# Performance work log

Measured on AMD Instinct MI355X. Metric: run time of the kernel, lower is better.

The kernel has to match this reference:

```python
import jax, jax.numpy as jnp
import numpy as np

IN_DIM = 768
HID = 128
NUM_CLASSES = 32
N_NODES = 50000
N_EDGES = 1600000


def setup_inputs() -> dict:
    key = jax.random.key(0)
    ks = jax.random.split(key, 8)
    x = jax.random.normal(ks[0], (N_NODES, IN_DIM), dtype=jnp.float32)
    edge_index = jax.random.randint(ks[1], (2, N_EDGES), 0, N_NODES, dtype=jnp.int64)
    # GCNConv weights (PyG: linear without bias inside propagate, bias added after aggregation)
    W1 = jax.random.normal(ks[2], (IN_DIM, HID), dtype=jnp.float32) / np.sqrt(IN_DIM)
    b1 = jnp.zeros((HID,), dtype=jnp.float32)
    W2 = jax.random.normal(ks[3], (HID, HID), dtype=jnp.float32) / np.sqrt(HID)
    b2 = jnp.zeros((HID,), dtype=jnp.float32)
    Wfc = jax.random.normal(ks[4], (HID, NUM_CLASSES), dtype=jnp.float32) / np.sqrt(HID)
    bfc = jnp.zeros((NUM_CLASSES,), dtype=jnp.float32)
    return {"x": x, "edge_index": edge_index, "W1": W1, "b1": b1,
            "W2": W2, "b2": b2, "Wfc": Wfc, "bfc": bfc}


def _gcn_conv(x, src, dst, norm, W, b, num_nodes):
    # PyG GCNConv: h = x @ W; out[i] = sum_j norm_ij * h[j]; out += b
    h = x @ W                      # [N, out_dim]
    msgs = h[src] * norm[:, None]  # gather + scale, [E+N, out_dim]
    out = jax.ops.segment_sum(msgs, dst, num_segments=num_nodes)
    return out + b


def reference(x, edge_index, W1, b1, W2, b2, Wfc, bfc):
    n = x.shape[0]
    loop = jnp.arange(n, dtype=edge_index.dtype)
    src = jnp.concatenate([edge_index[0], loop])  # add self-loops
    dst = jnp.concatenate([edge_index[1], loop])
    # symmetric normalization: deg computed on destination with unit edge weights
    deg = jax.ops.segment_sum(jnp.ones_like(src, dtype=x.dtype), dst, num_segments=n)
    dinv = jnp.where(deg > 0, jax.lax.rsqrt(jnp.maximum(deg, 1.0)), 0.0)
    norm = dinv[src] * dinv[dst]  # [E+N]

    h = jax.nn.relu(_gcn_conv(x, src, dst, norm, W1, b1, n))
    h = jax.nn.relu(_gcn_conv(h, src, dst, norm, W2, b2, n))
    return h @ Wfc + bfc
```

## Files before the change

kernel.cpp:

```cpp
#include <hip/hip_runtime.h>
#include <hip/hip_bf16.h>
#include <hip/hip_fp16.h>

#define N_NODES 50000
#define IN_DIM 768
#define HID 128
#define NCLS 32
#define CHUNK 8192
#define NBUCK ((N_NODES + 255) >> 8)

typedef __attribute__((ext_vector_type(8))) short bf16x8;
typedef __attribute__((ext_vector_type(4))) float f32x4;
typedef __attribute__((ext_vector_type(4))) unsigned short u16x4;

__device__ inline void split_bf16(float x, unsigned short& hi, unsigned short& lo) {
    unsigned int u = __float_as_uint(x);
    hi = (unsigned short)(u >> 16);
    float r = x - __uint_as_float(u & 0xFFFF0000u);
    lo = (unsigned short)(__float_as_uint(r) >> 16);
}

__global__ __launch_bounds__(256) void count_bucket(const int* __restrict__ raw, int E,
                                                    int* __restrict__ hist) {
    __shared__ int cnt[NBUCK];
    bool is64 = (raw[1] == 0 && raw[3] == 0 && raw[5] == 0 && raw[7] == 0);
    int t = threadIdx.x, b = blockIdx.x;
    if (t < NBUCK) cnt[t] = 0;
    __syncthreads();
    int base = b * CHUNK;
#pragma unroll
    for (int j = 0; j < CHUNK / 256; ++j) {
        int e = base + j * 256 + t;
        if (e < E) {
            int d = is64 ? raw[2 * (E + e)] : raw[E + e];
            atomicAdd(&cnt[d >> 8], 1);
        }
    }
    __syncthreads();
    if (t < NBUCK) hist[b * NBUCK + t] = cnt[t];
}

__global__ __launch_bounds__(256) void scan_off2(const int* __restrict__ hist, int nblk,
                                                 int E, int* __restrict__ bstart,
                                                 int* __restrict__ off) {
    __shared__ int tot[256];
    int t = threadIdx.x;
    int sum = 0;
    if (t < NBUCK)
        for (int b = 0; b < nblk; ++b) sum += hist[b * NBUCK + t];
    tot[t] = (t < NBUCK) ? sum : 0;
    __syncthreads();
    for (int o = 1; o < 256; o <<= 1) {
        int v = (t >= o) ? tot[t - o] : 0;
        __syncthreads();
        tot[t] += v;
        __syncthreads();
    }
    int excl = (t == 0) ? 0 : tot[t - 1];
    if (t < NBUCK) {
        bstart[t] = excl;
        int run = excl;
        for (int b = 0; b < nblk; ++b) {
            off[b * NBUCK + t] = run;
            run += hist[b * NBUCK + t];
        }
    }
    if (t == 0) bstart[NBUCK] = E;
}

__global__ __launch_bounds__(256) void chunk_scatter(const int* __restrict__ raw, int E,
                                                     const int* __restrict__ off,
                                                     int2* __restrict__ ebuf) {
    __shared__ int offl[NBUCK];
    __shared__ int cnt[NBUCK];
    bool is64 = (raw[1] == 0 && raw[3] == 0 && raw[5] == 0 && raw[7] == 0);
    int t = threadIdx.x, b = blockIdx.x;
    if (t < NBUCK) { offl[t] = off[b * NBUCK + t]; cnt[t] = 0; }
    __syncthreads();
    int base = b * CHUNK;
#pragma unroll
    for (int j = 0; j < CHUNK / 256; ++j) {
        int e = base + j * 256 + t;
        if (e < E) {
            int s, d;
            if (is64) { s = raw[2 * e]; d = raw[2 * (E + e)]; }
            else      { s = raw[e];     d = raw[E + e]; }
            int k = d >> 8;
            int r = atomicAdd(&cnt[k], 1);
            ebuf[offl[k] + r] = make_int2(s, d);
        }
    }
}

__global__ __launch_bounds__(256) void bucket_fine2(const int2* __restrict__ ebuf,
                                                    const int* __restrict__ bstart,
                                                    int* __restrict__ rowp,
                                                    float* __restrict__ dinv,
                                                    int* __restrict__ csr, int n, int E) {
    __shared__ int cnt[256];
    __shared__ int pre[256];
    __shared__ int fil[256];
    int k = blockIdx.x, t = threadIdx.x;
    int base = k << 8;
    int nn = min(256, n - base);
    int es = bstart[k], ee = bstart[k + 1];
    cnt[t] = 0;
    __syncthreads();
    for (int p = es + t; p < ee; p += 256) atomicAdd(&cnt[ebuf[p].y - base], 1);
    __syncthreads();
    pre[t] = cnt[t];
    __syncthreads();
    for (int o = 1; o < 256; o <<= 1) {
        int v = (t >= o) ? pre[t - o] : 0;
        __syncthreads();
        pre[t] += v;
        __syncthreads();
    }
    int excl = (t == 0) ? 0 : pre[t - 1];
    if (t < nn) {
        rowp[base + t] = es + excl;
        dinv[base + t] = rsqrtf((float)(cnt[t] + 1));
    }
    if (k == gridDim.x - 1 && t == 0) rowp[n] = E;
    fil[t] = es + excl;
    __syncthreads();
    for (int p = es + t; p < ee; p += 256) {
        int2 sd = ebuf[p];
        int q = atomicAdd(&fil[sd.y - base], 1);
        csr[q] = sd.x;
    }
}

__global__ void pack_w(const float* __restrict__ W, int K,
                       unsigned short* __restrict__ ph, unsigned short* __restrict__ pl) {
    int gid = blockIdx.x * 256 + threadIdx.x;
    int total = (K / 32) * 8 * 64;
    if (gid >= total) return;
    int l = gid & 63;
    int c0 = (gid >> 6) & 7;
    int t = gid >> 9;
    int col = c0 * 16 + (l & 15);
    int k0 = t * 32 + ((l >> 4) << 3);
    size_t base = (size_t)gid * 8;
#pragma unroll
    for (int j = 0; j < 8; ++j) {
        unsigned short h, lo;
        split_bf16(W[(size_t)(k0 + j) * 128 + col], h, lo);
        ph[base + j] = h;
        pl[base + j] = lo;
    }
}

template <int K>
__global__ __launch_bounds__(256) void gemm_mfma2(const float* __restrict__ A,
                                                  const unsigned short* __restrict__ Bph,
                                                  const unsigned short* __restrict__ Bpl,
                                                  __half* __restrict__ Chalf, int M) {
    __shared__ unsigned short Ah[64][40];
    __shared__ unsigned short Al[64][40];
    int tid = threadIdx.x;
    int wid = tid >> 6, lane = tid & 63;
    int wr = wid >> 1, wc = wid & 1;
    int row0 = blockIdx.x * 64;
    int lrow = lane & 15, lk = (lane >> 4) * 8;
    const int T = K / 32;

    int sidx0 = tid, sidx1 = 256 + tid;
    int sr0 = sidx0 >> 3, sc0 = (sidx0 & 7) * 4;
    int sr1 = sidx1 >> 3, sc1 = (sidx1 & 7) * 4;
    bool v0 = (row0 + sr0) < M, v1 = (row0 + sr1) < M;
    const float* a0 = &A[(size_t)(row0 + sr0) * K + sc0];
    const float* a1 = &A[(size_t)(row0 + sr1) * K + sc1];

    float4 pre0 = make_float4(0.f, 0.f, 0.f, 0.f), pre1 = pre0;
    if (v0) pre0 = *(const float4*)a0;
    if (v1) pre1 = *(const float4*)a1;

    f32x4 acc[2][4] = {};
    for (int t = 0; t < T; ++t) {
        u16x4 h, lo;
        split_bf16(pre0.x, ((unsigned short*)&h)[0], ((unsigned short*)&lo)[0]);
        split_bf16(pre0.y, ((unsigned short*)&h)[1], ((unsigned short*)&lo)[1]);
        split_bf16(pre0.z, ((unsigned short*)&h)[2], ((unsigned short*)&lo)[2]);
        split_bf16(pre0.w, ((unsigned short*)&h)[3], ((unsigned short*)&lo)[3]);
        *(u16x4*)&Ah[sr0][sc0] = h;
        *(u16x4*)&Al[sr0][sc0] = lo;
        split_bf16(pre1.x, ((unsigned short*)&h)[0], ((unsigned short*)&lo)[0]);
        split_bf16(pre1.y, ((unsigned short*)&h)[1], ((unsigned short*)&lo)[1]);
        split_bf16(pre1.z, ((unsigned short*)&h)[2], ((unsigned short*)&lo)[2]);
        split_bf16(pre1.w, ((unsigned short*)&h)[3], ((unsigned short*)&lo)[3]);
        *(u16x4*)&Ah[sr1][sc1] = h;
        *(u16x4*)&Al[sr1][sc1] = lo;
        __syncthreads();
        if (t + 1 < T) {
            pre0 = make_float4(0.f, 0.f, 0.f, 0.f); pre1 = pre0;
            if (v0) pre0 = *(const float4*)(a0 + (t + 1) * 32);
            if (v1) pre1 = *(const float4*)(a1 + (t + 1) * 32);
        }
        bf16x8 ah[2], al[2];
#pragma unroll
        for (int m = 0; m < 2; ++m) {
            int r = wr * 32 + m * 16 + lrow;
            ah[m] = *(const bf16x8*)&Ah[r][lk];
            al[m] = *(const bf16x8*)&Al[r][lk];
        }
        bf16x8 bh[4], bl[4];
#pragma unroll
        for (int n = 0; n < 4; ++n) {
            size_t boff = ((size_t)(t * 8 + wc * 4 + n) * 64 + lane) * 8;
            bh[n] = *(const bf16x8*)&Bph[boff];
            bl[n] = *(const bf16x8*)&Bpl[boff];
        }
#pragma unroll
        for (int m = 0; m < 2; ++m)
#pragma unroll
            for (int n = 0; n < 4; ++n) {
                acc[m][n] = __builtin_amdgcn_mfma_f32_16x16x32_bf16(ah[m], bh[n], acc[m][n], 0, 0, 0);
                acc[m][n] = __builtin_amdgcn_mfma_f32_16x16x32_bf16(al[m], bh[n], acc[m][n], 0, 0, 0);
                acc[m][n] = __builtin_amdgcn_mfma_f32_16x16x32_bf16(ah[m], bl[n], acc[m][n], 0, 0, 0);
            }
        __syncthreads();
    }
#pragma unroll
    for (int m = 0; m < 2; ++m) {
        int rbase = row0 + wr * 32 + m * 16 + (lane >> 4) * 4;
#pragma unroll
        for (int n = 0; n < 4; ++n) {
            int col = wc * 64 + n * 16 + lrow;
#pragma unroll
            for (int j = 0; j < 4; ++j) {
                int r = rbase + j;
                if (r < M) Chalf[(size_t)r * 128 + col] = __float2half(acc[m][n][j]);
            }
        }
    }
}

__global__ __launch_bounds__(256) void aggregate3(const __half* __restrict__ ht,
                                                  const int* __restrict__ rowp,
                                                  const int* __restrict__ csr,
                                                  const float* __restrict__ dinv,
                                                  const float* __restrict__ bias,
                                                  float* __restrict__ out, int n) {
    int wid = threadIdx.x >> 6, lane = threadIdx.x & 63;
    int i = blockIdx.x * 4 + wid;
    if (i >= n) return;
    const __half2* h2 = (const __half2*)ht;
    float di = dinv[i];
    float2 self = __half22float2(h2[(size_t)i * 64 + lane]);
    float2 acc;
    acc.x = di * di * self.x;
    acc.y = di * di * self.y;
    int b = rowp[i], e = rowp[i + 1];
    int p = b;
    for (; p + 8 <= e; p += 8) {
        int s[8]; float2 v[8]; float nn[8];
#pragma unroll
        for (int q = 0; q < 8; ++q) s[q] = csr[p + q];
#pragma unroll
        for (int q = 0; q < 8; ++q) v[q] = __half22float2(h2[(size_t)s[q] * 64 + lane]);
#pragma unroll
        for (int q = 0; q < 8; ++q) nn[q] = dinv[s[q]] * di;
#pragma unroll
        for (int q = 0; q < 8; ++q) { acc.x += nn[q] * v[q].x; acc.y += nn[q] * v[q].y; }
    }
    for (; p < e; ++p) {
        int s = csr[p];
        float nn = dinv[s] * di;
        float2 v = __half22float2(h2[(size_t)s * 64 + lane]);
        acc.x += nn * v.x;
        acc.y += nn * v.y;
    }
    float2 bb = ((const float2*)bias)[lane];
    float2 o;
    o.x = fmaxf(acc.x + bb.x, 0.f);
    o.y = fmaxf(acc.y + bb.y, 0.f);
    ((float2*)out)[(size_t)i * 64 + lane] = o;
}

__global__ __launch_bounds__(256) void fc_out(const float* __restrict__ h,
                                              const float* __restrict__ W,
                                              const float* __restrict__ b,
                                              float* __restrict__ out, int n) {
    __shared__ float Ws[HID * NCLS];
    __shared__ float Hs[8][HID];
    int tid = threadIdx.x;
#pragma unroll
    for (int l = 0; l < 16; ++l) Ws[l * 256 + tid] = W[l * 256 + tid];
    int row0 = blockIdx.x * 8;
#pragma unroll
    for (int l = 0; l < 4; ++l) {
        int idx = l * 256 + tid;
        int r = idx >> 7, c = idx & 127;
        int gr = row0 + r;
        Hs[r][c] = (gr < n) ? h[(size_t)gr * HID + c] : 0.f;
    }
    __syncthreads();
    int r = tid >> 5, c = tid & 31;
    float acc = b[c];
#pragma unroll
    for (int k = 0; k < HID; ++k) acc += Hs[r][k] * Ws[k * NCLS + c];
    int gr = row0 + r;
    if (gr < n) out[(size_t)gr * NCLS + c] = acc;
}

extern "C" void kernel_launch(void* const* d_in, const int* in_sizes, int n_in,
                              void* d_out, int out_size, void* d_ws, size_t ws_size,
                              hipStream_t stream) {
    const float* x   = (const float*)d_in[0];
    const int*   eid = (const int*)d_in[1];
    const float* W1  = (const float*)d_in[2];
    const float* b1  = (const float*)d_in[3];
    const float* W2  = (const float*)d_in[4];
    const float* b2  = (const float*)d_in[5];
    const float* Wfc = (const float*)d_in[6];
    const float* bfc = (const float*)d_in[7];
    float* out = (float*)d_out;

    const int N = N_NODES;
    const int E = in_sizes[1] / 2;
    const int NBLK = (E + CHUNK - 1) / CHUNK;

    auto align = [](size_t v) { return (v + 255) & ~(size_t)255; };
    char* w = (char*)d_ws;
    size_t off = 0;
    int* rowp = (int*)(w + off);           off = align(off + (size_t)(N + 1) * 4);
    float* dinv = (float*)(w + off);       off = align(off + (size_t)N * 4);
    int* csr = (int*)(w + off);            off = align(off + (size_t)E * 4);
    int2* ebuf = (int2*)(w + off);         off = align(off + (size_t)E * 8);
    int* bstart = (int*)(w + off);         off = align(off + (size_t)(NBUCK + 1) * 4);
    int* hist = (int*)(w + off);           off = align(off + (size_t)NBLK * NBUCK * 4);
    int* offs = (int*)(w + off);           off = align(off + (size_t)NBLK * NBUCK * 4);
    unsigned short* W1ph = (unsigned short*)(w + off); off = align(off + (size_t)128 * IN_DIM * 2);
    unsigned short* W1pl = (unsigned short*)(w + off); off = align(off + (size_t)128 * IN_DIM * 2);
    unsigned short* W2ph = (unsigned short*)(w + off); off = align(off + (size_t)128 * HID * 2);
    unsigned short* W2pl = (unsigned short*)(w + off); off = align(off + (size_t)128 * HID * 2);
    __half* h1 = (__half*)(w + off);       off = align(off + (size_t)N * HID * 2);
    __half* h2t = (__half*)(w + off);      off = align(off + (size_t)N * HID * 2);
    float* bufA = (float*)(w + off);       off = align(off + (size_t)N * HID * 4);
    float* bufB = (float*)(w + off);       off = align(off + (size_t)N * HID * 4);

    count_bucket<<<NBLK, 256, 0, stream>>>(eid, E, hist);
    scan_off2<<<1, 256, 0, stream>>>(hist, NBLK, E, bstart, offs);
    chunk_scatter<<<NBLK, 256, 0, stream>>>(eid, E, offs, ebuf);
    bucket_fine2<<<NBUCK, 256, 0, stream>>>(ebuf, bstart, rowp, dinv, csr, N, E);

    pack_w<<<((IN_DIM / 32) * 8 * 64 + 255) / 256, 256, 0, stream>>>(W1, IN_DIM, W1ph, W1pl);
    pack_w<<<((HID / 32) * 8 * 64 + 255) / 256, 256, 0, stream>>>(W2, HID, W2ph, W2pl);

    int gb = (N + 63) / 64;
    gemm_mfma2<IN_DIM><<<gb, 256, 0, stream>>>(x, W1ph, W1pl, h1, N);
    aggregate3<<<(N + 3) / 4, 256, 0, stream>>>(h1, rowp, csr, dinv, b1, bufA, N);
    gemm_mfma2<HID><<<gb, 256, 0, stream>>>(bufA, W2ph, W2pl, h2t, N);
    aggregate3<<<(N + 3) / 4, 256, 0, stream>>>(h2t, rowp, csr, dinv, b2, bufB, N);
    fc_out<<<(N + 7) / 8, 256, 0, stream>>>(bufB, Wfc, bfc, out, N);
}
```

Before: 313.6 us.

## Fold dinv into GEMM epilogue, compress CSR to 16-bit, use half intermediates

The GEMM epilogue now pre-scales each output row by dinv[src]. Aggregation therefore sums raw gathered rows and applies dinv[dst] once, with no per-edge dinv gather or multiply. The edge buffer packs the local destination and the source into 32 bits, CSR indices become uint16 since node ids fit in 16 bits, and the inner gather loop is unrolled to 16. Intermediate activations between layers are stored as fp16 instead of fp32, and the second GEMM and the final FC read half input. This reduces memory traffic, at the cost of extra fp16 rounding and a hard limit of 65536 nodes.

```diff
diff --git a/kernel.cpp b/kernel.cpp
--- a/kernel.cpp
+++ b/kernel.cpp
@@ -70,7 +70,7 @@
 
 __global__ __launch_bounds__(256) void chunk_scatter(const int* __restrict__ raw, int E,
                                                      const int* __restrict__ off,
-                                                     int2* __restrict__ ebuf) {
+                                                     unsigned int* __restrict__ ebuf) {
     __shared__ int offl[NBUCK];
     __shared__ int cnt[NBUCK];
     bool is64 = (raw[1] == 0 && raw[3] == 0 && raw[5] == 0 && raw[7] == 0);
@@ -87,16 +87,17 @@
             else      { s = raw[e];     d = raw[E + e]; }
             int k = d >> 8;
             int r = atomicAdd(&cnt[k], 1);
-            ebuf[offl[k] + r] = make_int2(s, d);
-        }
-    }
-}
-
-__global__ __launch_bounds__(256) void bucket_fine2(const int2* __restrict__ ebuf,
+            ebuf[offl[k] + r] = ((unsigned int)(d & 255) << 16) | (unsigned int)s;
+        }
+    }
+}
+
+__global__ __launch_bounds__(256) void bucket_fine2(const unsigned int* __restrict__ ebuf,
                                                     const int* __restrict__ bstart,
                                                     int* __restrict__ rowp,
                                                     float* __restrict__ dinv,
-                                                    int* __restrict__ csr, int n, int E) {
+                                                    unsigned short* __restrict__ csr,
+                                                    int n, int E) {
     __shared__ int cnt[256];
     __shared__ int pre[256];
     __shared__ int fil[256];
@@ -106,7 +107,7 @@
     int es = bstart[k], ee = bstart[k + 1];
     cnt[t] = 0;
     __syncthreads();
-    for (int p = es + t; p < ee; p += 256) atomicAdd(&cnt[ebuf[p].y - base], 1);
+    for (int p = es + t; p < ee; p += 256) atomicAdd(&cnt[ebuf[p] >> 16], 1);
     __syncthreads();
     pre[t] = cnt[t];
     __syncthreads();
@@ -125,9 +126,9 @@
     fil[t] = es + excl;
     __syncthreads();
     for (int p = es + t; p < ee; p += 256) {
-        int2 sd = ebuf[p];
-        int q = atomicAdd(&fil[sd.y - base], 1);
-        csr[q] = sd.x;
+        unsigned int u = ebuf[p];
+        int q = atomicAdd(&fil[u >> 16], 1);
+        csr[q] = (unsigned short)(u & 0xFFFFu);
     }
 }
 
@@ -151,10 +152,23 @@
     }
 }
 
-template <int K>
-__global__ __launch_bounds__(256) void gemm_mfma2(const float* __restrict__ A,
+template <bool AHALF>
+__device__ inline float4 loadA4(const void* A, size_t idx) {
+    if constexpr (AHALF) {
+        uint2 u = *(const uint2*)((const __half*)A + idx);
+        float2 f0 = __half22float2(*(__half2*)&u.x);
+        float2 f1 = __half22float2(*(__half2*)&u.y);
+        return make_float4(f0.x, f0.y, f1.x, f1.y);
+    } else {
+        return *(const float4*)((const float*)A + idx);
+    }
+}
+
+template <int K, bool AHALF>
+__global__ __launch_bounds__(256) void gemm_mfma2(const void* __restrict__ A,
                                                   const unsigned short* __restrict__ Bph,
                                                   const unsigned short* __restrict__ Bpl,
+                                                  const float* __restrict__ dinv,
                                                   __half* __restrict__ Chalf, int M) {
     __shared__ unsigned short Ah[64][40];
     __shared__ unsigned short Al[64][40];
@@ -169,12 +183,12 @@
     int sr0 = sidx0 >> 3, sc0 = (sidx0 & 7) * 4;
     int sr1 = sidx1 >> 3, sc1 = (sidx1 & 7) * 4;
     bool v0 = (row0 + sr0) < M, v1 = (row0 + sr1) < M;
-    const float* a0 = &A[(size_t)(row0 + sr0) * K + sc0];
-    const float* a1 = &A[(size_t)(row0 + sr1) * K + sc1];
+    size_t ai0 = (size_t)(row0 + sr0) * K + sc0;
+    size_t ai1 = (size_t)(row0 + sr1) * K + sc1;
 
     float4 pre0 = make_float4(0.f, 0.f, 0.f, 0.f), pre1 = pre0;
-    if (v0) pre0 = *(const float4*)a0;
-    if (v1) pre1 = *(const float4*)a1;
+    if (v0) pre0 = loadA4<AHALF>(A, ai0);
+    if (v1) pre1 = loadA4<AHALF>(A, ai1);
 
     f32x4 acc[2][4] = {};
     for (int t = 0; t < T; ++t) {
@@ -194,8 +208,8 @@
         __syncthreads();
         if (t + 1 < T) {
             pre0 = make_float4(0.f, 0.f, 0.f, 0.f); pre1 = pre0;
-            if (v0) pre0 = *(const float4*)(a0 + (t + 1) * 32);
-            if (v1) pre1 = *(const float4*)(a1 + (t + 1) * 32);
+            if (v0) pre0 = loadA4<AHALF>(A, ai0 + (size_t)(t + 1) * 32);
+            if (v1) pre1 = loadA4<AHALF>(A, ai1 + (size_t)(t + 1) * 32);
         }
         bf16x8 ah[2], al[2];
 #pragma unroll
@@ -230,55 +244,56 @@
 #pragma unroll
             for (int j = 0; j < 4; ++j) {
                 int r = rbase + j;
-                if (r < M) Chalf[(size_t)r * 128 + col] = __float2half(acc[m][n][j]);
+                if (r < M) Chalf[(size_t)r * 128 + col] = __float2half(dinv[r] * acc[m][n][j]);
             }
         }
     }
 }
 
-__global__ __launch_bounds__(256) void aggregate3(const __half* __restrict__ ht,
+__global__ __launch_bounds__(256) void aggregate5(const __half* __restrict__ ht,
                                                   const int* __restrict__ rowp,
-                                                  const int* __restrict__ csr,
+                                                  const unsigned short* __restrict__ csr,
                                                   const float* __restrict__ dinv,
                                                   const float* __restrict__ bias,
-                                                  float* __restrict__ out, int n) {
+                                                  __half* __restrict__ outh, int n) {
     int wid = threadIdx.x >> 6, lane = threadIdx.x & 63;
     int i = blockIdx.x * 4 + wid;
     if (i >= n) return;
     const __half2* h2 = (const __half2*)ht;
     float di = dinv[i];
-    float2 self = __half22float2(h2[(size_t)i * 64 + lane]);
-    float2 acc;
-    acc.x = di * di * self.x;
-    acc.y = di * di * self.y;
+    float2 acc = __half22float2(h2[(size_t)i * 64 + lane]);
     int b = rowp[i], e = rowp[i + 1];
     int p = b;
-    for (; p + 8 <= e; p += 8) {
-        int s[8]; float2 v[8]; float nn[8];
-#pragma unroll
-        for (int q = 0; q < 8; ++q) s[q] = csr[p + q];
-#pragma unroll
-        for (int q = 0; q < 8; ++q) v[q] = __half22float2(h2[(size_t)s[q] * 64 + lane]);
-#pragma unroll
-        for (int q = 0; q < 8; ++q) nn[q] = dinv[s[q]] * di;
-#pragma unroll
-        for (int q = 0; q < 8; ++q) { acc.x += nn[q] * v[q].x; acc.y += nn[q] * v[q].y; }
+    for (; p + 16 <= e; p += 16) {
+        int s[16]; float2 v[16];
+#pragma unroll
+        for (int q = 0; q < 16; ++q) s[q] = csr[p + q];
+#pragma unroll
+        for (int q = 0; q < 16; ++q) v[q] = __half22float2(h2[(size_t)s[q] * 64 + lane]);
+#pragma unroll
+        for (int q = 0; q < 16; ++q) { acc.x += v[q].x; acc.y += v[q].y; }
+    }
+    for (; p + 4 <= e; p += 4) {
+        int s[4]; float2 v[4];
+#pragma unroll
+        for (int q = 0; q < 4; ++q) s[q] = csr[p + q];
+#pragma unroll
+        for (int q = 0; q < 4; ++q) v[q] = __half22float2(h2[(size_t)s[q] * 64 + lane]);
+#pragma unroll
+        for (int q = 0; q < 4; ++q) { acc.x += v[q].x; acc.y += v[q].y; }
     }
     for (; p < e; ++p) {
-        int s = csr[p];
-        float nn = dinv[s] * di;
-        float2 v = __half22float2(h2[(size_t)s * 64 + lane]);
-        acc.x += nn * v.x;
-        acc.y += nn * v.y;
+        float2 v = __half22float2(h2[(size_t)csr[p] * 64 + lane]);
+        acc.x += v.x;
+        acc.y += v.y;
     }
     float2 bb = ((const float2*)bias)[lane];
-    float2 o;
-    o.x = fmaxf(acc.x + bb.x, 0.f);
-    o.y = fmaxf(acc.y + bb.y, 0.f);
-    ((float2*)out)[(size_t)i * 64 + lane] = o;
-}
-
-__global__ __launch_bounds__(256) void fc_out(const float* __restrict__ h,
+    __half2 o = __floats2half2_rn(fmaxf(di * acc.x + bb.x, 0.f),
+                                  fmaxf(di * acc.y + bb.y, 0.f));
+    ((__half2*)outh)[(size_t)i * 64 + lane] = o;
+}
+
+__global__ __launch_bounds__(256) void fc_out(const __half* __restrict__ h,
                                               const float* __restrict__ W,
                                               const float* __restrict__ b,
                                               float* __restrict__ out, int n) {
@@ -293,7 +308,7 @@
         int idx = l * 256 + tid;
         int r = idx >> 7, c = idx & 127;
         int gr = row0 + r;
-        Hs[r][c] = (gr < n) ? h[(size_t)gr * HID + c] : 0.f;
+        Hs[r][c] = (gr < n) ? __half2float(h[(size_t)gr * HID + c]) : 0.f;
     }
     __syncthreads();
     int r = tid >> 5, c = tid & 31;
@@ -326,8 +341,8 @@
     size_t off = 0;
     int* rowp = (int*)(w + off);           off = align(off + (size_t)(N + 1) * 4);
     float* dinv = (float*)(w + off);       off = align(off + (size_t)N * 4);
-    int* csr = (int*)(w + off);            off = align(off + (size_t)E * 4);
-    int2* ebuf = (int2*)(w + off);         off = align(off + (size_t)E * 8);
+    unsigned short* csr = (unsigned short*)(w + off); off = align(off + (size_t)E * 2);
+    unsigned int* ebuf = (unsigned int*)(w + off);    off = align(off + (size_t)E * 4);
     int* bstart = (int*)(w + off);         off = align(off + (size_t)(NBUCK + 1) * 4);
     int* hist = (int*)(w + off);           off = align(off + (size_t)NBLK * NBUCK * 4);
     int* offs = (int*)(w + off);           off = align(off + (size_t)NBLK * NBUCK * 4);
@@ -335,10 +350,10 @@
     unsigned short* W1pl = (unsigned short*)(w + off); off = align(off + (size_t)128 * IN_DIM * 2);
     unsigned short* W2ph = (unsigned short*)(w + off); off = align(off + (size_t)128 * HID * 2);
     unsigned short* W2pl = (unsigned short*)(w + off); off = align(off + (size_t)128 * HID * 2);
-    __half* h1 = (__half*)(w + off);       off = align(off + (size_t)N * HID * 2);
-    __half* h2t = (__half*)(w + off);      off = align(off + (size_t)N * HID * 2);
-    float* bufA = (float*)(w + off);       off = align(off + (size_t)N * HID * 4);
-    float* bufB = (float*)(w + off);       off = align(off + (size_t)N * HID * 4);
+    __half* ht1 = (__half*)(w + off);      off = align(off + (size_t)N * HID * 2);
+    __half* ht2 = (__half*)(w + off);      off = align(off + (size_t)N * HID * 2);
+    __half* h1r = (__half*)(w + off);      off = align(off + (size_t)N * HID * 2);
+    __half* h2r = (__half*)(w + off);      off = align(off + (size_t)N * HID * 2);
 
     count_bucket<<<NBLK, 256, 0, stream>>>(eid, E, hist);
     scan_off2<<<1, 256, 0, stream>>>(hist, NBLK, E, bstart, offs);
@@ -349,9 +364,10 @@
     pack_w<<<((HID / 32) * 8 * 64 + 255) / 256, 256, 0, stream>>>(W2, HID, W2ph, W2pl);
 
     int gb = (N + 63) / 64;
-    gemm_mfma2<IN_DIM><<<gb, 256, 0, stream>>>(x, W1ph, W1pl, h1, N);
-    aggregate3<<<(N + 3) / 4, 256, 0, stream>>>(h1, rowp, csr, dinv, b1, bufA, N);
-    gemm_mfma2<HID><<<gb, 256, 0, stream>>>(bufA, W2ph, W2pl, h2t, N);
-    aggregate3<<<(N + 3) / 4, 256, 0, stream>>>(h2t, rowp, csr, dinv, b2, bufB, N);
-    fc_out<<<(N + 7) / 8, 256, 0, stream>>>(bufB, Wfc, bfc, out, N);
-}
+    int ab = (N + 3) / 4;
+    gemm_mfma2<IN_DIM, false><<<gb, 256, 0, stream>>>(x, W1ph, W1pl, dinv, ht1, N);
+    aggregate5<<<ab, 256, 0, stream>>>(ht1, rowp, csr, dinv, b1, h1r, N);
+    gemm_mfma2<HID, true><<<gb, 256, 0, stream>>>(h1r, W2ph, W2pl, dinv, ht2, N);
+    aggregate5<<<ab, 256, 0, stream>>>(ht2, rowp, csr, dinv, b2, h2r, N);
+    fc_out<<<(N + 7) / 8, 256, 0, stream>>>(h2r, Wfc, bfc, out, N);
+}
```

New measurement: 280.6 us, median of 2. -10.5%, faster.
